# Performance work log

Hardware: AMD Instinct MI355X
Metric: run time of the kernel (lower is better)

Reference implementation:

```python
import jax, jax.numpy as jnp
import numpy as np

B, N, F_NODE, F_EDGE, F_G = 2, 512, 128, 16, 128
MID, OUT = 128, 128


def _linear_params(key, fan_in, fan_out):
    kw, kb = jax.random.split(key)
    scale = 1.0 / np.sqrt(fan_in)
    W = jax.random.normal(kw, (fan_in, fan_out), dtype=jnp.float32) * scale
    b = jnp.zeros((fan_out,), dtype=jnp.float32)
    return W, b


def setup_inputs() -> dict:
    key = jax.random.key(0)
    ks = jax.random.split(key, 12)
    features = jax.random.normal(ks[0], (B, N, F_NODE), dtype=jnp.float32)
    e_features = jax.random.normal(ks[1], (B, N, N, F_EDGE), dtype=jnp.float32)
    g_features = jax.random.normal(ks[2], (B, F_G), dtype=jnp.float32)
    adj = jax.random.randint(ks[3], (B, N, N), 0, 2).astype(jnp.float32)
    W1, b1 = _linear_params(ks[4], F_NODE, MID)
    W2, b2 = _linear_params(ks[5], F_NODE, MID)
    We, be = _linear_params(ks[6], F_EDGE, MID)
    Wg, bg = _linear_params(ks[7], F_G, MID)
    Wo1, bo1 = _linear_params(ks[8], F_NODE, OUT)
    Wo2, bo2 = _linear_params(ks[9], MID, OUT)
    return dict(features=features, e_features=e_features, g_features=g_features,
                adj=adj, W1=W1, b1=b1, W2=W2, b2=b2, We=We, be=be, Wg=Wg, bg=bg,
                Wo1=Wo1, bo1=bo1, Wo2=Wo2, bo2=bo2)


def reference(features, e_features, g_features, adj,
              W1, b1, W2, b2, We, be, Wg, bg, Wo1, bo1, Wo2, bo2):
    # Linear projections (haiku Linear = xW + b)
    msg_1 = jnp.einsum('bnf,fm->bnm', features, W1) + b1      # (b,n,mid)
    msg_2 = jnp.einsum('bnf,fm->bnm', features, W2) + b2      # (b,n,mid)
    msg_e = jnp.einsum('bije,em->bijm', e_features, We) + be  # (b,n,n,mid)
    msg_g = jnp.einsum('bg,gm->bm', g_features, Wg) + bg      # (b,mid)
    # All-pairs broadcast sum: (b,n,n,mid)
    msgs = (msg_1[:, None, :, :] + msg_2[:, :, None, :]
            + msg_e + msg_g[:, None, None, :])
    # Masked max reduction over axis=1 (default reduction=jnp.max)
    msgs = jnp.max(msgs * adj[..., None], axis=1)             # (b,n,mid)
    h_1 = jnp.einsum('bnf,fo->bno', features, Wo1) + bo1
    h_2 = jnp.einsum('bnm,mo->bno', msgs, Wo2) + bo2
    return h_1 + h_2
```

## Files before the change

### kernel.cpp

```cpp
#include <hip/hip_runtime.h>
#include <hip/hip_bf16.h>
#include <math.h>

#define B_   2
#define N_   512
#define FN   128
#define FE   16
#define MID_ 128

typedef __attribute__((ext_vector_type(8)))  short short8_t;
typedef __attribute__((ext_vector_type(16))) float f32x16;

__device__ __forceinline__ short f2bf(float f) {
    __bf16 h = (__bf16)f;
    return __builtin_bit_cast(short, h);
}
__device__ __forceinline__ unsigned enc_f32(float f) {
    unsigned u = __float_as_uint(f);
    return u ^ (0x80000000u | (unsigned)((int)u >> 31));
}
__device__ __forceinline__ float dec_f32(unsigned u) {
    unsigned m = (u & 0x80000000u) ? 0x80000000u : 0xFFFFFFFFu;
    return __uint_as_float(u ^ m);
}
#define ENC_NEG_INF 0x007FFFFFu

__global__ __launch_bounds__(256) void kA(
    const float* __restrict__ feat, const float* __restrict__ gfeat,
    const float* __restrict__ W1, const float* __restrict__ b1,
    const float* __restrict__ W2, const float* __restrict__ b2,
    const float* __restrict__ be,
    const float* __restrict__ Wg, const float* __restrict__ bg,
    const float* __restrict__ Wo1, const float* __restrict__ bo1,
    float* __restrict__ msg1c, float* __restrict__ msg2, float* __restrict__ h1)
{
    __shared__ float fl[2 * 128];
    const int bid = blockIdx.x;
    const int b   = bid >> 8;
    const int n0  = (bid & 255) * 2;
    const int t   = threadIdx.x;
    const int r   = t >> 7, m = t & 127;

    const float* fbase = feat + (size_t)(b * N_ + n0) * FN;
    if (t < 64) ((float4*)fl)[t] = ((const float4*)fbase)[t];
    __syncthreads();

    float mg = bg[m] + be[m];
    for (int k = 0; k < FN; ++k) mg += gfeat[b * FN + k] * Wg[k * MID_ + m];

    float a1 = 0.f, a2 = 0.f, a3 = 0.f;
    for (int k = 0; k < FN; ++k) {
        const float f = fl[r * 128 + k];
        a1 += f * W1[k * MID_ + m];
        a2 += f * W2[k * MID_ + m];
        a3 += f * Wo1[k * MID_ + m];
    }
    const size_t idx = (size_t)(b * N_ + n0 + r) * MID_ + m;
    msg1c[idx] = a1 + b1[m] + mg;
    msg2[idx]  = a2 + b2[m];
    h1[idx]    = a3 + bo1[m];
}

__global__ __launch_bounds__(512, 2) void kB(
    const float* __restrict__ ef, const float* __restrict__ adj,
    const float* __restrict__ We,
    const float* __restrict__ msg1c, const float* __restrict__ msg2,
    unsigned* __restrict__ part)
{
    __shared__ float    adj_l[64 * 32];
    __shared__ unsigned tile[32 * 128];

    const int bid = blockIdx.x;
    const int b   = bid >> 7;
    const int jt  = (bid >> 3) & 15;
    const int ic  = bid & 7;
    const int j0  = jt * 32, i0 = ic * 64;
    const int t   = threadIdx.x;
    const int wid = t >> 6;
    const int g   = (t >> 5) & 1;
    const int lm  = t & 31;

    {
        const int il = t >> 3, joff = (t & 7) * 4;
        *(float4*)&adj_l[il * 32 + joff] =
            *(const float4*)(adj + (size_t)(b * N_ + i0 + il) * N_ + j0 + joff);
    }
    #pragma unroll
    for (int q = 0; q < 8; ++q) tile[t + q * 512] = ENC_NEG_INF;

    short8_t Bf[4];
    #pragma unroll
    for (int mt = 0; mt < 4; ++mt) {
        short8_t s;
        #pragma unroll
        for (int j = 0; j < 8; ++j)
            s[j] = f2bf(We[(8 * g + j) * MID_ + mt * 32 + lm]);
        Bf[mt] = s;
    }
    float c1f[4][16];
    #pragma unroll
    for (int mt = 0; mt < 4; ++mt)
        #pragma unroll
        for (int r = 0; r < 16; ++r) {
            const int jr = (r & 3) + 8 * (r >> 2) + 4 * g;
            c1f[mt][r] = msg1c[(size_t)(b * N_ + j0 + jr) * MID_ + mt * 32 + lm];
        }

    float accm[4][16];
    #pragma unroll
    for (int mt = 0; mt < 4; ++mt)
        #pragma unroll
        for (int r = 0; r < 16; ++r) accm[mt][r] = -INFINITY;

    __syncthreads();

    const int iw0 = i0 + wid * 8;
    for (int ii = 0; ii < 8; ++ii) {
        const int i  = iw0 + ii;
        const int il = wid * 8 + ii;
        const float* efr = ef + ((size_t)(b * N_ + i) * N_ + j0 + lm) * FE + 8 * g;
        const float4 ea = *(const float4*)efr;
        const float4 eb = *(const float4*)(efr + 4);
        short8_t Af;
        Af[0] = f2bf(ea.x); Af[1] = f2bf(ea.y); Af[2] = f2bf(ea.z); Af[3] = f2bf(ea.w);
        Af[4] = f2bf(eb.x); Af[5] = f2bf(eb.y); Af[6] = f2bf(eb.z); Af[7] = f2bf(eb.w);
        float af[16];
        #pragma unroll
        for (int r = 0; r < 16; ++r)
            af[r] = adj_l[il * 32 + (r & 3) + 8 * (r >> 2) + 4 * g];

        #pragma unroll
        for (int mt = 0; mt < 4; ++mt) {
            const float m2v = msg2[(size_t)(b * N_ + i) * MID_ + mt * 32 + lm];
            f32x16 C;
            #pragma unroll
            for (int r = 0; r < 16; ++r) C[r] = c1f[mt][r] + m2v;
            const f32x16 S = __builtin_amdgcn_mfma_f32_32x32x16_bf16(Af, Bf[mt], C, 0, 0, 0);
            #pragma unroll
            for (int r = 0; r < 16; ++r)
                accm[mt][r] = fmaxf(accm[mt][r], S[r] * af[r]);
        }
    }

    #pragma unroll
    for (int mt = 0; mt < 4; ++mt)
        #pragma unroll
        for (int r = 0; r < 16; ++r) {
            const int idx = ((r & 3) + 8 * (r >> 2) + 4 * g) * MID_ + mt * 32 + lm;
            atomicMax(&tile[idx], enc_f32(accm[mt][r]));
        }
    __syncthreads();

    unsigned* dst = part + ((size_t)(ic * 2 + b) * N_ + j0) * MID_;
    #pragma unroll
    for (int q = 0; q < 2; ++q)
        ((uint4*)dst)[t * 2 + q] = ((const uint4*)tile)[t * 2 + q];
}

__global__ __launch_bounds__(256) void kC(
    const unsigned* __restrict__ part, const float* __restrict__ h1,
    const float* __restrict__ Wo2, const float* __restrict__ bo2,
    float* __restrict__ out)
{
    __shared__ float ms[2 * 128];
    const int bid = blockIdx.x;
    const int b   = bid >> 8;
    const int j0  = (bid & 255) * 2;
    const int t   = threadIdx.x;
    const int r   = t >> 7, m = t & 127;
    const int j   = j0 + r;

    unsigned u = ENC_NEG_INF;
    #pragma unroll
    for (int icc = 0; icc < 8; ++icc) {
        const unsigned p = part[((size_t)(icc * 2 + b) * N_ + j) * MID_ + m];
        u = (p > u) ? p : u;
    }
    ms[r * 128 + m] = dec_f32(u);
    __syncthreads();

    const int o = m;
    float acc = h1[(size_t)(b * N_ + j) * MID_ + o] + bo2[o];
    for (int k = 0; k < MID_; ++k)
        acc += ms[r * 128 + k] * Wo2[k * MID_ + o];
    out[(size_t)(b * N_ + j) * MID_ + o] = acc;
}

extern "C" void kernel_launch(void* const* d_in, const int* in_sizes, int n_in,
                              void* d_out, int out_size, void* d_ws, size_t ws_size,
                              hipStream_t stream)
{
    const float* feat = (const float*)d_in[0];
    const float* ef   = (const float*)d_in[1];
    const float* gf   = (const float*)d_in[2];
    const float* adj  = (const float*)d_in[3];
    const float* W1   = (const float*)d_in[4];
    const float* b1   = (const float*)d_in[5];
    const float* W2   = (const float*)d_in[6];
    const float* b2   = (const float*)d_in[7];
    const float* We   = (const float*)d_in[8];
    const float* be   = (const float*)d_in[9];
    const float* Wg   = (const float*)d_in[10];
    const float* bg   = (const float*)d_in[11];
    const float* Wo1  = (const float*)d_in[12];
    const float* bo1  = (const float*)d_in[13];
    const float* Wo2  = (const float*)d_in[14];
    const float* bo2  = (const float*)d_in[15];
    float* out = (float*)d_out;

    float*    ws    = (float*)d_ws;
    float*    msg1c = ws;
    float*    msg2  = ws + 131072;
    float*    h1    = ws + 262144;
    unsigned* part  = (unsigned*)(ws + 393216);

    hipLaunchKernelGGL(kA, dim3(512), dim3(256), 0, stream,
        feat, gf, W1, b1, W2, b2, be, Wg, bg, Wo1, bo1, msg1c, msg2, h1);
    hipLaunchKernelGGL(kB, dim3(256), dim3(512), 0, stream,
        ef, adj, We, msg1c, msg2, part);
    hipLaunchKernelGGL(kC, dim3(512), dim3(256), 0, stream,
        part, h1, Wo2, bo2, out);
}
```

Before: 36.95 us.

## Restructure all three kernels: smaller i-tiles, LDS edge staging, adjacency bitmask, vectorized GEMVs

The edge kernel now uses 32x32 (i,j) tiles over 512 blocks. Edge features are staged into swizzled LDS as bf16, and adjacency becomes a ballot bitmask that folds the mask into the MFMA accumulator init as -inf. msg1c is added once after the max instead of every iteration, and the LDS atomicMax tile is replaced by a two-wave-group merge. The projection and output kernels move to float4/float2 vectorized weight loads with more rows per block. Together these aim to cut redundant global loads, per-element multiply by adj, and atomics. The cost is more partial buffers (16 i-chunks) to reduce in kC, plus a reworked mask semantics that must reproduce zero for masked entries via anyzf.

Result: slower. 145.2 us (+292.9%).

```diff
diff --git a/kernel.cpp b/kernel.cpp
--- a/kernel.cpp
+++ b/kernel.cpp
@@ -34,127 +34,152 @@
     const float* __restrict__ Wo1, const float* __restrict__ bo1,
     float* __restrict__ msg1c, float* __restrict__ msg2, float* __restrict__ h1)
 {
-    __shared__ float fl[2 * 128];
+    __shared__ float fl[32 * FN];
     const int bid = blockIdx.x;
-    const int b   = bid >> 8;
-    const int n0  = (bid & 255) * 2;
+    const int b   = bid >> 6;
+    const int nt  = (bid >> 2) & 15;
+    const int mq  = bid & 3;
+    const int n0  = nt * 32;
     const int t   = threadIdx.x;
-    const int r   = t >> 7, m = t & 127;
-
-    const float* fbase = feat + (size_t)(b * N_ + n0) * FN;
-    if (t < 64) ((float4*)fl)[t] = ((const float4*)fbase)[t];
-    __syncthreads();
-
-    float mg = bg[m] + be[m];
-    for (int k = 0; k < FN; ++k) mg += gfeat[b * FN + k] * Wg[k * MID_ + m];
-
-    float a1 = 0.f, a2 = 0.f, a3 = 0.f;
+    const int row = t >> 3;
+    const int m0  = mq * 32 + (t & 7) * 4;
+
+    const float4* fsrc = (const float4*)(feat + (size_t)(b * N_ + n0) * FN);
+    #pragma unroll
+    for (int q = 0; q < 4; ++q) ((float4*)fl)[t + 256 * q] = fsrc[t + 256 * q];
+    __syncthreads();
+
+    float a1x=0,a1y=0,a1z=0,a1w=0, a2x=0,a2y=0,a2z=0,a2w=0;
+    float a3x=0,a3y=0,a3z=0,a3w=0, mgx=0,mgy=0,mgz=0,mgw=0;
+    #pragma unroll 4
     for (int k = 0; k < FN; ++k) {
-        const float f = fl[r * 128 + k];
-        a1 += f * W1[k * MID_ + m];
-        a2 += f * W2[k * MID_ + m];
-        a3 += f * Wo1[k * MID_ + m];
-    }
-    const size_t idx = (size_t)(b * N_ + n0 + r) * MID_ + m;
-    msg1c[idx] = a1 + b1[m] + mg;
-    msg2[idx]  = a2 + b2[m];
-    h1[idx]    = a3 + bo1[m];
-}
-
-__global__ __launch_bounds__(512, 2) void kB(
+        const float f   = fl[row * FN + k];
+        const float gfk = gfeat[b * FN + k];
+        const float4 w1 = *(const float4*)&W1 [k * MID_ + m0];
+        const float4 w2 = *(const float4*)&W2 [k * MID_ + m0];
+        const float4 w3 = *(const float4*)&Wo1[k * MID_ + m0];
+        const float4 wg = *(const float4*)&Wg [k * MID_ + m0];
+        a1x += f*w1.x; a1y += f*w1.y; a1z += f*w1.z; a1w += f*w1.w;
+        a2x += f*w2.x; a2y += f*w2.y; a2z += f*w2.z; a2w += f*w2.w;
+        a3x += f*w3.x; a3y += f*w3.y; a3z += f*w3.z; a3w += f*w3.w;
+        mgx += gfk*wg.x; mgy += gfk*wg.y; mgz += gfk*wg.z; mgw += gfk*wg.w;
+    }
+    const float4 b1v = *(const float4*)&b1 [m0];
+    const float4 b2v = *(const float4*)&b2 [m0];
+    const float4 bev = *(const float4*)&be [m0];
+    const float4 bgv = *(const float4*)&bg [m0];
+    const float4 bov = *(const float4*)&bo1[m0];
+    const size_t idx = (size_t)(b * N_ + n0 + row) * MID_ + m0;
+    float4 o;
+    o.x = a1x + b1v.x + mgx + bgv.x + bev.x;
+    o.y = a1y + b1v.y + mgy + bgv.y + bev.y;
+    o.z = a1z + b1v.z + mgz + bgv.z + bev.z;
+    o.w = a1w + b1v.w + mgw + bgv.w + bev.w;
+    *(float4*)&msg1c[idx] = o;
+    o.x = a2x + b2v.x; o.y = a2y + b2v.y; o.z = a2z + b2v.z; o.w = a2w + b2v.w;
+    *(float4*)&msg2[idx] = o;
+    o.x = a3x + bov.x; o.y = a3y + bov.y; o.z = a3z + bov.z; o.w = a3w + bov.w;
+    *(float4*)&h1[idx] = o;
+}
+
+__global__ __launch_bounds__(512, 4) void kB(
     const float* __restrict__ ef, const float* __restrict__ adj,
     const float* __restrict__ We,
     const float* __restrict__ msg1c, const float* __restrict__ msg2,
     unsigned* __restrict__ part)
 {
-    __shared__ float    adj_l[64 * 32];
-    __shared__ unsigned tile[32 * 128];
+    __shared__ __align__(16) unsigned short efl[32 * 32 * 16];
+    __shared__ unsigned madj[32];
+    __shared__ float    anyzf[32];
+    __shared__ float    mtile[4][32 * 32];
 
     const int bid = blockIdx.x;
-    const int b   = bid >> 7;
-    const int jt  = (bid >> 3) & 15;
-    const int ic  = bid & 7;
-    const int j0  = jt * 32, i0 = ic * 64;
-    const int t   = threadIdx.x;
-    const int wid = t >> 6;
-    const int g   = (t >> 5) & 1;
-    const int lm  = t & 31;
+    const int b   = bid >> 8;
+    const int jt  = (bid >> 4) & 15;
+    const int ic  = bid & 15;
+    const int j0  = jt * 32, i0 = ic * 32;
+    const int t    = threadIdx.x;
+    const int lane = t & 63, wid = t >> 6;
+    const int mt   = wid & 3, ih = wid >> 2;
+    const int g    = lane >> 5, lm = lane & 31;
 
     {
-        const int il = t >> 3, joff = (t & 7) * 4;
-        *(float4*)&adj_l[il * 32 + joff] =
-            *(const float4*)(adj + (size_t)(b * N_ + i0 + il) * N_ + j0 + joff);
-    }
-    #pragma unroll
-    for (int q = 0; q < 8; ++q) tile[t + q * 512] = ENC_NEG_INF;
-
-    short8_t Bf[4];
-    #pragma unroll
-    for (int mt = 0; mt < 4; ++mt) {
-        short8_t s;
-        #pragma unroll
-        for (int j = 0; j < 8; ++j)
-            s[j] = f2bf(We[(8 * g + j) * MID_ + mt * 32 + lm]);
-        Bf[mt] = s;
-    }
-    float c1f[4][16];
-    #pragma unroll
-    for (int mt = 0; mt < 4; ++mt)
+        const int i_l = t >> 4;
+        const float4* src = (const float4*)(ef + ((size_t)(b * N_ + i0 + i_l) * N_ + j0) * FE);
+        #pragma unroll
+        for (int q = 0; q < 8; ++q) {
+            const int p = (t & 15) + 16 * q;
+            const float4 v = src[p];
+            const int j = p >> 2, e0 = (p & 3) * 4;
+            short4 sv;
+            sv.x = f2bf(v.x); sv.y = f2bf(v.y); sv.z = f2bf(v.z); sv.w = f2bf(v.w);
+            const int hidx = ((i_l * 32 + j) * 16 + e0) ^ ((j & 4) << 1);
+            *(short4*)&efl[hidx] = sv;
+        }
+    }
+    #pragma unroll
+    for (int p = 0; p < 2; ++p) {
+        const int i_l = wid * 4 + 2 * p + g;
+        const float av = adj[(size_t)(b * N_ + i0 + i_l) * N_ + j0 + lm];
+        const unsigned long long bal = __ballot(av != 0.0f);
+        if (lane == 0)  madj[i_l] = (unsigned)bal;
+        if (lane == 32) madj[i_l] = (unsigned)(bal >> 32);
+    }
+
+    short8_t Bf;
+    #pragma unroll
+    for (int jj = 0; jj < 8; ++jj)
+        Bf[jj] = f2bf(We[(8 * g + jj) * MID_ + mt * 32 + lm]);
+
+    f32x16 accm;
+    #pragma unroll
+    for (int r = 0; r < 16; ++r) accm[r] = -INFINITY;
+
+    __syncthreads();
+
+    if (t < 32) {
+        unsigned ao = 0xFFFFFFFFu;
+        for (int i2 = 0; i2 < 32; ++i2) ao &= madj[i2];
+        anyzf[t] = ((ao >> t) & 1u) ? -INFINITY : 0.0f;
+    }
+
+    const size_t m2base = (size_t)(b * N_ + i0) * MID_ + mt * 32 + lm;
+    #pragma unroll 4
+    for (int ii = 0; ii < 16; ++ii) {
+        const int i_l = ih * 16 + ii;
+        const int hh = ((i_l * 32 + lm) * 16 + 8 * g) ^ ((lm & 4) << 1);
+        const short8_t Af = *(const short8_t*)&efl[hh];
+        const float m2v = msg2[m2base + (size_t)i_l * MID_];
+        const unsigned vm = madj[i_l] >> (g * 4);
+        f32x16 C;
         #pragma unroll
         for (int r = 0; r < 16; ++r) {
-            const int jr = (r & 3) + 8 * (r >> 2) + 4 * g;
-            c1f[mt][r] = msg1c[(size_t)(b * N_ + j0 + jr) * MID_ + mt * 32 + lm];
-        }
-
-    float accm[4][16];
-    #pragma unroll
-    for (int mt = 0; mt < 4; ++mt)
-        #pragma unroll
-        for (int r = 0; r < 16; ++r) accm[mt][r] = -INFINITY;
-
-    __syncthreads();
-
-    const int iw0 = i0 + wid * 8;
-    for (int ii = 0; ii < 8; ++ii) {
-        const int i  = iw0 + ii;
-        const int il = wid * 8 + ii;
-        const float* efr = ef + ((size_t)(b * N_ + i) * N_ + j0 + lm) * FE + 8 * g;
-        const float4 ea = *(const float4*)efr;
-        const float4 eb = *(const float4*)(efr + 4);
-        short8_t Af;
-        Af[0] = f2bf(ea.x); Af[1] = f2bf(ea.y); Af[2] = f2bf(ea.z); Af[3] = f2bf(ea.w);
-        Af[4] = f2bf(eb.x); Af[5] = f2bf(eb.y); Af[6] = f2bf(eb.z); Af[7] = f2bf(eb.w);
-        float af[16];
-        #pragma unroll
-        for (int r = 0; r < 16; ++r)
-            af[r] = adj_l[il * 32 + (r & 3) + 8 * (r >> 2) + 4 * g];
-
-        #pragma unroll
-        for (int mt = 0; mt < 4; ++mt) {
-            const float m2v = msg2[(size_t)(b * N_ + i) * MID_ + mt * 32 + lm];
-            f32x16 C;
-            #pragma unroll
-            for (int r = 0; r < 16; ++r) C[r] = c1f[mt][r] + m2v;
-            const f32x16 S = __builtin_amdgcn_mfma_f32_32x32x16_bf16(Af, Bf[mt], C, 0, 0, 0);
-            #pragma unroll
-            for (int r = 0; r < 16; ++r)
-                accm[mt][r] = fmaxf(accm[mt][r], S[r] * af[r]);
-        }
-    }
-
-    #pragma unroll
-    for (int mt = 0; mt < 4; ++mt)
+            const int cr = (r & 3) + 8 * (r >> 2);
+            C[r] = (vm & (1u << cr)) ? m2v : -INFINITY;
+        }
+        const f32x16 S = __builtin_amdgcn_mfma_f32_32x32x16_bf16(Af, Bf, C, 0, 0, 0);
+        #pragma unroll
+        for (int r = 0; r < 16; ++r) accm[r] = fmaxf(accm[r], S[r]);
+    }
+
+    if (ih == 1) {
         #pragma unroll
         for (int r = 0; r < 16; ++r) {
-            const int idx = ((r & 3) + 8 * (r >> 2) + 4 * g) * MID_ + mt * 32 + lm;
-            atomicMax(&tile[idx], enc_f32(accm[mt][r]));
-        }
-    __syncthreads();
-
-    unsigned* dst = part + ((size_t)(ic * 2 + b) * N_ + j0) * MID_;
-    #pragma unroll
-    for (int q = 0; q < 2; ++q)
-        ((uint4*)dst)[t * 2 + q] = ((const uint4*)tile)[t * 2 + q];
+            const int jrow = (r & 3) + 8 * (r >> 2) + 4 * g;
+            mtile[mt][jrow * 32 + lm] = accm[r];
+        }
+    }
+    __syncthreads();
+    if (ih == 0) {
+        #pragma unroll
+        for (int r = 0; r < 16; ++r) {
+            const int jrow = (r & 3) + 8 * (r >> 2) + 4 * g;
+            float v = fmaxf(accm[r], mtile[mt][jrow * 32 + lm]);
+            v += msg1c[(size_t)(b * N_ + j0 + jrow) * MID_ + mt * 32 + lm];
+            v = fmaxf(v, anyzf[jrow]);
+            part[((size_t)(ic * 2 + b) * N_ + j0 + jrow) * MID_ + mt * 32 + lm] = enc_f32(v);
+        }
+    }
 }
 
 __global__ __launch_bounds__(256) void kC(
@@ -162,28 +187,38 @@
     const float* __restrict__ Wo2, const float* __restrict__ bo2,
     float* __restrict__ out)
 {
-    __shared__ float ms[2 * 128];
+    __shared__ float ms[4 * MID_];
     const int bid = blockIdx.x;
-    const int b   = bid >> 8;
-    const int j0  = (bid & 255) * 2;
+    const int b   = bid >> 7;
+    const int j0  = (bid & 127) * 4;
     const int t   = threadIdx.x;
-    const int r   = t >> 7, m = t & 127;
-    const int j   = j0 + r;
-
-    unsigned u = ENC_NEG_INF;
-    #pragma unroll
-    for (int icc = 0; icc < 8; ++icc) {
-        const unsigned p = part[((size_t)(icc * 2 + b) * N_ + j) * MID_ + m];
-        u = (p > u) ? p : u;
-    }
-    ms[r * 128 + m] = dec_f32(u);
-    __syncthreads();
-
-    const int o = m;
-    float acc = h1[(size_t)(b * N_ + j) * MID_ + o] + bo2[o];
-    for (int k = 0; k < MID_; ++k)
-        acc += ms[r * 128 + k] * Wo2[k * MID_ + o];
-    out[(size_t)(b * N_ + j) * MID_ + o] = acc;
+    {
+        const int v0 = t * 2;
+        const int r = v0 >> 7, m = v0 & 127;
+        const size_t base = ((size_t)b * N_ + j0 + r) * MID_ + m;
+        unsigned ua = ENC_NEG_INF, ub = ENC_NEG_INF;
+        #pragma unroll
+        for (int icc = 0; icc < 16; ++icc) {
+            const uint2 pv = *(const uint2*)&part[(size_t)icc * 2 * N_ * MID_ + base];
+            ua = pv.x > ua ? pv.x : ua;
+            ub = pv.y > ub ? pv.y : ub;
+        }
+        ms[v0] = dec_f32(ua); ms[v0 + 1] = dec_f32(ub);
+    }
+    __syncthreads();
+    const int r  = t >> 6, o0 = (t & 63) * 2;
+    const int j  = j0 + r;
+    const size_t hidx = (size_t)(b * N_ + j) * MID_ + o0;
+    float ax = h1[hidx]     + bo2[o0];
+    float ay = h1[hidx + 1] + bo2[o0 + 1];
+    #pragma unroll 4
+    for (int k = 0; k < MID_; ++k) {
+        const float msv = ms[r * MID_ + k];
+        const float2 w = *(const float2*)&Wo2[k * MID_ + o0];
+        ax += msv * w.x; ay += msv * w.y;
+    }
+    float2 res; res.x = ax; res.y = ay;
+    *(float2*)&out[hidx] = res;
 }
 
 extern "C" void kernel_launch(void* const* d_in, const int* in_sizes, int n_in,
@@ -214,10 +249,10 @@
     float*    h1    = ws + 262144;
     unsigned* part  = (unsigned*)(ws + 393216);
 
-    hipLaunchKernelGGL(kA, dim3(512), dim3(256), 0, stream,
+    hipLaunchKernelGGL(kA, dim3(128), dim3(256), 0, stream,
         feat, gf, W1, b1, W2, b2, be, Wg, bg, Wo1, bo1, msg1c, msg2, h1);
-    hipLaunchKernelGGL(kB, dim3(256), dim3(512), 0, stream,
+    hipLaunchKernelGGL(kB, dim3(512), dim3(512), 0, stream,
         ef, adj, We, msg1c, msg2, part);
-    hipLaunchKernelGGL(kC, dim3(512), dim3(256), 0, stream,
+    hipLaunchKernelGGL(kC, dim3(256), dim3(256), 0, stream,
         part, h1, Wo2, bo2, out);
 }
```
